# Kernel tuning notes

Measured on AMD Instinct MI355X. Metric: run time of the kernel, lower is better.

## Reference

```python
import jax, jax.numpy as jnp
import numpy as np

N, D_IN, D_OUT, Q_DIM = 4096, 256, 256, 64


def _xavier(key, shape):
    fan_in, fan_out = shape[-2], shape[-1]
    bound = float(np.sqrt(6.0 / (fan_in + fan_out)))
    return jax.random.uniform(key, shape, jnp.float32, -bound, bound)


def setup_inputs() -> dict:
    key = jax.random.key(0)
    k_x, k_q, k_w, k_b = jax.random.split(key, 4)
    x = jax.random.normal(k_x, (N, D_IN), jnp.float32)
    query_vectors = jax.random.normal(k_q, (N, Q_DIM), jnp.float32)
    W_1 = _xavier(k_w, (Q_DIM, D_IN, D_OUT))  # xavier over last two dims (matches torch on 3D)
    b_1 = _xavier(k_b, (Q_DIM, D_OUT))
    return {"x": x, "query_vectors": query_vectors, "W_1": W_1, "b_1": b_1}


def reference(x, query_vectors, W_1, b_1):
    # Per-sample dynamic weight: W[n] = sum_d q[n,d] * W_1[d]; then x[n] @ W[n] + q[n] @ b_1.
    # Fused single contraction avoids materializing the [n, i, o] tensor; same math.
    out = jnp.einsum('ni,nd,dio->no', x, query_vectors, W_1)
    out = out + query_vectors @ b_1
    return out
```

## Files before the change

kernel.cpp:

```cpp
#include <hip/hip_runtime.h>
#include <stdint.h>


typedef _Float16 f16;
typedef f16 f16x8 __attribute__((ext_vector_type(8)));
typedef float f32x16 __attribute__((ext_vector_type(16)));

#define NROWS 4096
#define QDIM 64
#define SPLIT 8
#define MBLK 64

__device__ __forceinline__ void gl_lds16(const void* g, void* s) {
  __builtin_amdgcn_global_load_lds(
      (const __attribute__((address_space(1))) void*)(uintptr_t)g,
      (__attribute__((address_space(3))) void*)(uint32_t)(uintptr_t)s,
      16, 0, 0);
}

__global__ __launch_bounds__(256) void prep(const float* __restrict__ W,
                                            const float* __restrict__ X,
                                            const float* __restrict__ Q,
                                            const float* __restrict__ B1,
                                            f16* __restrict__ Wt,
                                            f16* __restrict__ Xt,
                                            f16* __restrict__ Qt) {
  const int b = blockIdx.x;
  const int t = threadIdx.x;
  if (b < 512) {
    const int sg = b >> 6, ic = (b >> 3) & 7, dd = b & 7;
    const int g = b + (sg ? 2 : 0);
    const int k0 = ((sg << 3) + dd) * 256 + (ic << 5);
#pragma unroll
    for (int r = 0; r < 4; ++r) {
      const int gidx = (r << 8) + t;
      const int n = gidx & 255;
      const int sh = gidx >> 8;
      f16x8 h;
#pragma unroll
      for (int j = 0; j < 8; ++j)
        h[j] = (f16)W[(size_t)(k0 + (sh << 3) + j) * 256 + n];
      *(f16x8*)(Wt + (size_t)g * 8192 + (size_t)gidx * 8) = h;
    }
  } else if (b < 640) {
    const int bb = b - 512;
    const int mb = bb >> 1, half = bb & 1;
#pragma unroll
    for (int r = 0; r < 4; ++r) {
      const int gidx = (half << 10) + (r << 8) + t;
      const int row = gidx & 63;
      const int hsic = gidx >> 6;
      const float* src = X + (size_t)((mb << 6) + row) * 256 + (hsic << 3);
      float4 a = *(const float4*)src;
      float4 c = *(const float4*)(src + 4);
      f16x8 h;
      h[0] = (f16)a.x; h[1] = (f16)a.y; h[2] = (f16)a.z; h[3] = (f16)a.w;
      h[4] = (f16)c.x; h[5] = (f16)c.y; h[6] = (f16)c.z; h[7] = (f16)c.w;
      *(f16x8*)(Xt + (size_t)mb * 16384 + (size_t)gidx * 8) = h;
    }
  } else if (b < 656) {
    const int bb = b - 640;
#pragma unroll
    for (int m = 0; m < 4; ++m) {
      const int mb = (bb << 2) + m;
#pragma unroll
      for (int r = 0; r < 2; ++r) {
        const int u = (r << 8) + t;
        const int row = u & 63;
        const int sh = u >> 6;
        const float* src = Q + (size_t)((mb << 6) + row) * QDIM + (sh << 3);
        float4 a = *(const float4*)src;
        float4 c = *(const float4*)(src + 4);
        f16x8 h;
        h[0] = (f16)a.x; h[1] = (f16)a.y; h[2] = (f16)a.z; h[3] = (f16)a.w;
        h[4] = (f16)c.x; h[5] = (f16)c.y; h[6] = (f16)c.z; h[7] = (f16)c.w;
        *(f16x8*)(Qt + (size_t)mb * 4096 + (size_t)u * 8) = h;
      }
    }
  } else {
    const int cc = b - 656;
#pragma unroll
    for (int r = 0; r < 4; ++r) {
      const int gidx = (r << 8) + t;
      const int n = gidx & 255;
      const int sh = gidx >> 8;
      f16x8 h;
#pragma unroll
      for (int j = 0; j < 8; ++j)
        h[j] = (f16)B1[(size_t)((cc << 5) + (sh << 3) + j) * 256 + n];
      *(f16x8*)(Wt + (size_t)(64 + cc) * 8192 + (size_t)gidx * 8) = h;
    }
  }
}

__global__ __launch_bounds__(256, 2) void mlp_main(const float* __restrict__ Q,
                                                   const f16* __restrict__ Wt,
                                                   const f16* __restrict__ Xt,
                                                   const f16* __restrict__ Qt,
                                                   float* __restrict__ out) {
  __shared__ f16 s_x[16384];
  __shared__ f16 s_w[4][3][2048];

  const int bid = blockIdx.x;
  const int sg = bid & 7;
  const int mb = bid >> 3;
  const int t = threadIdx.x;
  const int w = t >> 6;
  const int l = t & 63;
  const int l31 = l & 31;
  const int hf = l >> 5;
  const int chunks = (sg == 0) ? 66 : 64;
  const char* wg = (const char*)(Wt + (size_t)((sg << 6) + (sg ? 2 : 0)) * 8192);

  const char* xg = (const char*)(Xt + (size_t)mb * 16384);
  char* xs = (char*)s_x;
#pragma unroll
  for (int i = 0; i < 8; ++i) {
    const int off = (((w << 3) + i) << 10) + (l << 4);
    gl_lds16(xg + off, xs + off);
  }
  char* ws0 = (char*)&s_w[w][0][0];
#pragma unroll
  for (int c0 = 0; c0 < 2; ++c0)
#pragma unroll
    for (int i = 0; i < 4; ++i)
      gl_lds16(wg + ((size_t)c0 << 14) + (i << 12) + (w << 10) + (l << 4),
               ws0 + (c0 << 12) + (i << 10) + (l << 4));

  f16 qr[2][8];
#pragma unroll
  for (int mt = 0; mt < 2; ++mt) {
    const float* qp = Q + (size_t)((mb << 6) + (mt << 5) + l31) * QDIM + (sg << 3);
#pragma unroll
    for (int dd = 0; dd < 8; ++dd) qr[mt][dd] = (f16)qp[dd];
  }

  f16x8 qf[2][2][2];
  if (sg == 0) {
#pragma unroll
    for (int cc = 0; cc < 2; ++cc)
#pragma unroll
      for (int mt = 0; mt < 2; ++mt)
#pragma unroll
        for (int s = 0; s < 2; ++s)
          qf[cc][mt][s] = *(const f16x8*)(Qt + (size_t)mb * 4096 +
              (size_t)(((((cc << 1) + s) << 1) + hf) * 64 + (mt << 5) + l31) * 8);
  }

  f32x16 acc[2][2];
#pragma unroll
  for (int a = 0; a < 2; ++a)
#pragma unroll
    for (int bq = 0; bq < 2; ++bq)
#pragma unroll
      for (int r = 0; r < 16; ++r) acc[a][bq][r] = 0.f;

  __syncthreads();

  const int wrd = (hf << 10) + (l31 << 4);
  const char* rb = ws0;
  const char* pb = ws0 + 4096;
  char* fb = ws0 + 8192;
  int pc = 2;

  for (int ic = 0; ic < 8; ++ic) {
    f16x8 xf[2][2];
#pragma unroll
    for (int s = 0; s < 2; ++s)
#pragma unroll
      for (int mt = 0; mt < 2; ++mt)
        xf[mt][s] = *(const f16x8*)(s_x +
            ((((ic << 2) + (s << 1) + hf) << 6) + (mt << 5) + l31) * 8);
#pragma unroll
    for (int dd = 0; dd < 8; ++dd) {
      const char* src = wg + ((size_t)pc << 14);
#pragma unroll
      for (int i = 0; i < 4; ++i)
        gl_lds16(src + (i << 12) + (w << 10) + (l << 4),
                 fb + (i << 10) + (l << 4));
      pc = (pc + 1 < chunks) ? pc + 1 : 0;
      const f16 qa0 = qr[0][dd], qa1 = qr[1][dd];
      f16x8 a00 = xf[0][0] * qa0, a10 = xf[1][0] * qa1;
      f16x8 a01 = xf[0][1] * qa0, a11 = xf[1][1] * qa1;
      __builtin_amdgcn_s_waitcnt(0x0F78);
      __builtin_amdgcn_sched_barrier(0);
      f16x8 bf00 = *(const f16x8*)(rb + wrd);
      f16x8 bf01 = *(const f16x8*)(rb + wrd + (1 << 9));
      f16x8 bf10 = *(const f16x8*)(rb + (2 << 10) + wrd);
      f16x8 bf11 = *(const f16x8*)(rb + (2 << 10) + wrd + (1 << 9));
      acc[0][0] = __builtin_amdgcn_mfma_f32_32x32x16_f16(a00, bf00, acc[0][0], 0, 0, 0);
      acc[1][0] = __builtin_amdgcn_mfma_f32_32x32x16_f16(a10, bf00, acc[1][0], 0, 0, 0);
      acc[0][1] = __builtin_amdgcn_mfma_f32_32x32x16_f16(a00, bf01, acc[0][1], 0, 0, 0);
      acc[1][1] = __builtin_amdgcn_mfma_f32_32x32x16_f16(a10, bf01, acc[1][1], 0, 0, 0);
      acc[0][0] = __builtin_amdgcn_mfma_f32_32x32x16_f16(a01, bf10, acc[0][0], 0, 0, 0);
      acc[1][0] = __builtin_amdgcn_mfma_f32_32x32x16_f16(a11, bf10, acc[1][0], 0, 0, 0);
      acc[0][1] = __builtin_amdgcn_mfma_f32_32x32x16_f16(a01, bf11, acc[0][1], 0, 0, 0);
      acc[1][1] = __builtin_amdgcn_mfma_f32_32x32x16_f16(a11, bf11, acc[1][1], 0, 0, 0);
      const char* tmp = rb; rb = pb; pb = fb; fb = (char*)tmp;
    }
  }

  if (sg == 0) {
#pragma unroll
    for (int cc = 0; cc < 2; ++cc) {
      const char* src = wg + ((size_t)pc << 14);
#pragma unroll
      for (int i = 0; i < 4; ++i)
        gl_lds16(src + (i << 12) + (w << 10) + (l << 4),
                 fb + (i << 10) + (l << 4));
      pc = (pc + 1 < chunks) ? pc + 1 : 0;
      __builtin_amdgcn_s_waitcnt(0x0F78);
      __builtin_amdgcn_sched_barrier(0);
      f16x8 bf00 = *(const f16x8*)(rb + wrd);
      f16x8 bf01 = *(const f16x8*)(rb + wrd + (1 << 9));
      f16x8 bf10 = *(const f16x8*)(rb + (2 << 10) + wrd);
      f16x8 bf11 = *(const f16x8*)(rb + (2 << 10) + wrd + (1 << 9));
      acc[0][0] = __builtin_amdgcn_mfma_f32_32x32x16_f16(qf[cc][0][0], bf00, acc[0][0], 0, 0, 0);
      acc[1][0] = __builtin_amdgcn_mfma_f32_32x32x16_f16(qf[cc][1][0], bf00, acc[1][0], 0, 0, 0);
      acc[0][1] = __builtin_amdgcn_mfma_f32_32x32x16_f16(qf[cc][0][0], bf01, acc[0][1], 0, 0, 0);
      acc[1][1] = __builtin_amdgcn_mfma_f32_32x32x16_f16(qf[cc][1][0], bf01, acc[1][1], 0, 0, 0);
      acc[0][0] = __builtin_amdgcn_mfma_f32_32x32x16_f16(qf[cc][0][1], bf10, acc[0][0], 0, 0, 0);
      acc[1][0] = __builtin_amdgcn_mfma_f32_32x32x16_f16(qf[cc][1][1], bf10, acc[1][0], 0, 0, 0);
      acc[0][1] = __builtin_amdgcn_mfma_f32_32x32x16_f16(qf[cc][0][1], bf11, acc[0][1], 0, 0, 0);
      acc[1][1] = __builtin_amdgcn_mfma_f32_32x32x16_f16(qf[cc][1][1], bf11, acc[1][1], 0, 0, 0);
      const char* tmp = rb; rb = pb; pb = fb; fb = (char*)tmp;
    }
  }

  __builtin_amdgcn_s_waitcnt(0x0F70);

#pragma unroll
  for (int mt = 0; mt < 2; ++mt) {
#pragma unroll
    for (int nt = 0; nt < 2; ++nt) {
#pragma unroll
      for (int r = 0; r < 16; ++r) {
        const int row = (mb << 6) + (mt << 5) + (r & 3) + ((r >> 2) << 3) + (hf << 2);
        const int col = (w << 6) + (nt << 5) + l31;
        atomicAdd(out + (size_t)row * 256 + col, acc[mt][nt][r]);
      }
    }
  }
}

extern "C" void kernel_launch(void* const* d_in, const int* in_sizes, int n_in,
                              void* d_out, int out_size, void* d_ws, size_t ws_size,
                              hipStream_t stream) {
  (void)in_sizes; (void)n_in; (void)out_size; (void)ws_size;
  const float* x  = (const float*)d_in[0];
  const float* q  = (const float*)d_in[1];
  const float* W1 = (const float*)d_in[2];
  const float* b1 = (const float*)d_in[3];
  float* out = (float*)d_out;

  f16* Wt = (f16*)d_ws;
  f16* Xt = (f16*)((char*)d_ws + (size_t)514 * 16384);
  f16* Qt = (f16*)((char*)d_ws + (size_t)514 * 16384 + (size_t)64 * 32768);

  hipMemsetAsync(out, 0, (size_t)NROWS * 256 * sizeof(float), stream);
  prep<<<658, 256, 0, stream>>>(W1, x, q, b1, Wt, Xt, Qt);
  mlp_main<<<(NROWS / MBLK) * SPLIT, 256, 0, stream>>>(q, Wt, Xt, Qt, out);
}
```

Baseline: 132.5 us.

## Load W and X fragments directly to registers, dropping LDS staging

Removes the shared-memory staging of X and W chunks (global_load_lds with triple buffering and waitcnt) and loads the MFMA operand fragments straight from global memory into registers. It uses a register double-buffer for W and for X, and raises launch bounds to 3 blocks per SM since no LDS is used. This cuts LDS traffic and explicit sync, and relies on the compiler and cache hierarchy to hide global latency. The trade-off is higher register pressure and dependence on L2/L1 for reuse of X across loops.

```diff
diff --git a/kernel.cpp b/kernel.cpp
--- a/kernel.cpp
+++ b/kernel.cpp
@@ -10,13 +10,6 @@
 #define QDIM 64
 #define SPLIT 8
 #define MBLK 64
-
-__device__ __forceinline__ void gl_lds16(const void* g, void* s) {
-  __builtin_amdgcn_global_load_lds(
-      (const __attribute__((address_space(1))) void*)(uintptr_t)g,
-      (__attribute__((address_space(3))) void*)(uint32_t)(uintptr_t)s,
-      16, 0, 0);
-}
 
 __global__ __launch_bounds__(256) void prep(const float* __restrict__ W,
                                             const float* __restrict__ X,
@@ -93,14 +86,55 @@
   }
 }
 
-__global__ __launch_bounds__(256, 2) void mlp_main(const float* __restrict__ Q,
+#define LOADW(D, P)                          \
+  do {                                       \
+    D[0] = *(const f16x8*)((P));             \
+    D[1] = *(const f16x8*)((P) + 512);       \
+    D[2] = *(const f16x8*)((P) + 8192);      \
+    D[3] = *(const f16x8*)((P) + 8704);      \
+  } while (0)
+
+#define LOADX(D, IC)                               \
+  do {                                             \
+    const char* xb_ = xg + ((IC) << 12);           \
+    D[0] = *(const f16x8*)(xb_);                   \
+    D[1] = *(const f16x8*)(xb_ + 512);             \
+    D[2] = *(const f16x8*)(xb_ + 2048);            \
+    D[3] = *(const f16x8*)(xb_ + 2560);            \
+  } while (0)
+
+#define MFMA8(XF, DD, WW)                                                        \
+  do {                                                                           \
+    const f16 q0_ = qr[0][DD], q1_ = qr[1][DD];                                  \
+    f16x8 a00_ = XF[0] * q0_, a10_ = XF[1] * q1_;                                \
+    f16x8 a01_ = XF[2] * q0_, a11_ = XF[3] * q1_;                                \
+    acc[0][0] = __builtin_amdgcn_mfma_f32_32x32x16_f16(a00_, WW[0], acc[0][0], 0, 0, 0); \
+    acc[1][0] = __builtin_amdgcn_mfma_f32_32x32x16_f16(a10_, WW[0], acc[1][0], 0, 0, 0); \
+    acc[0][1] = __builtin_amdgcn_mfma_f32_32x32x16_f16(a00_, WW[1], acc[0][1], 0, 0, 0); \
+    acc[1][1] = __builtin_amdgcn_mfma_f32_32x32x16_f16(a10_, WW[1], acc[1][1], 0, 0, 0); \
+    acc[0][0] = __builtin_amdgcn_mfma_f32_32x32x16_f16(a01_, WW[2], acc[0][0], 0, 0, 0); \
+    acc[1][0] = __builtin_amdgcn_mfma_f32_32x32x16_f16(a11_, WW[2], acc[1][0], 0, 0, 0); \
+    acc[0][1] = __builtin_amdgcn_mfma_f32_32x32x16_f16(a01_, WW[3], acc[0][1], 0, 0, 0); \
+    acc[1][1] = __builtin_amdgcn_mfma_f32_32x32x16_f16(a11_, WW[3], acc[1][1], 0, 0, 0); \
+  } while (0)
+
+#define MFMA8Q(QF, WW)                                                           \
+  do {                                                                           \
+    acc[0][0] = __builtin_amdgcn_mfma_f32_32x32x16_f16(QF[0], WW[0], acc[0][0], 0, 0, 0); \
+    acc[1][0] = __builtin_amdgcn_mfma_f32_32x32x16_f16(QF[1], WW[0], acc[1][0], 0, 0, 0); \
+    acc[0][1] = __builtin_amdgcn_mfma_f32_32x32x16_f16(QF[0], WW[1], acc[0][1], 0, 0, 0); \
+    acc[1][1] = __builtin_amdgcn_mfma_f32_32x32x16_f16(QF[1], WW[1], acc[1][1], 0, 0, 0); \
+    acc[0][0] = __builtin_amdgcn_mfma_f32_32x32x16_f16(QF[2], WW[2], acc[0][0], 0, 0, 0); \
+    acc[1][0] = __builtin_amdgcn_mfma_f32_32x32x16_f16(QF[3], WW[2], acc[1][0], 0, 0, 0); \
+    acc[0][1] = __builtin_amdgcn_mfma_f32_32x32x16_f16(QF[2], WW[3], acc[0][1], 0, 0, 0); \
+    acc[1][1] = __builtin_amdgcn_mfma_f32_32x32x16_f16(QF[3], WW[3], acc[1][1], 0, 0, 0); \
+  } while (0)
+
+__global__ __launch_bounds__(256, 3) void mlp_main(const float* __restrict__ Q,
                                                    const f16* __restrict__ Wt,
                                                    const f16* __restrict__ Xt,
                                                    const f16* __restrict__ Qt,
                                                    float* __restrict__ out) {
-  __shared__ f16 s_x[16384];
-  __shared__ f16 s_w[4][3][2048];
-
   const int bid = blockIdx.x;
   const int sg = bid & 7;
   const int mb = bid >> 3;
@@ -109,23 +143,12 @@
   const int l = t & 63;
   const int l31 = l & 31;
   const int hf = l >> 5;
-  const int chunks = (sg == 0) ? 66 : 64;
+
   const char* wg = (const char*)(Wt + (size_t)((sg << 6) + (sg ? 2 : 0)) * 8192);
-
-  const char* xg = (const char*)(Xt + (size_t)mb * 16384);
-  char* xs = (char*)s_x;
-#pragma unroll
-  for (int i = 0; i < 8; ++i) {
-    const int off = (((w << 3) + i) << 10) + (l << 4);
-    gl_lds16(xg + off, xs + off);
-  }
-  char* ws0 = (char*)&s_w[w][0][0];
-#pragma unroll
-  for (int c0 = 0; c0 < 2; ++c0)
-#pragma unroll
-    for (int i = 0; i < 4; ++i)
-      gl_lds16(wg + ((size_t)c0 << 14) + (i << 12) + (w << 10) + (l << 4),
-               ws0 + (c0 << 12) + (i << 10) + (l << 4));
+  const int wl = (hf << 12) + (w << 10) + (l31 << 4);
+  const char* cp = wg + wl;
+
+  const char* xg = (const char*)Xt + ((size_t)mb << 15) + (hf << 10) + (l31 << 4);
 
   f16 qr[2][8];
 #pragma unroll
@@ -135,99 +158,53 @@
     for (int dd = 0; dd < 8; ++dd) qr[mt][dd] = (f16)qp[dd];
   }
 
-  f16x8 qf[2][2][2];
+  f32x16 acc[2][2];
+#pragma unroll
+  for (int a = 0; a < 2; ++a)
+#pragma unroll
+    for (int bq = 0; bq < 2; ++bq)
+#pragma unroll
+      for (int r = 0; r < 16; ++r) acc[a][bq][r] = 0.f;
+
+  f16x8 WA[4], WB[4], xfA[4], xfB[4];
+
+  LOADW(WA, cp);
+  LOADX(xfA, 0);
+
+  for (int ic2 = 0; ic2 < 4; ++ic2) {
+    LOADX(xfB, (ic2 << 1) + 1);
+#pragma unroll
+    for (int p = 0; p < 4; ++p) {
+      LOADW(WB, cp + 16384);
+      MFMA8(xfA, (p << 1), WA);
+      LOADW(WA, cp + 32768);
+      MFMA8(xfA, (p << 1) + 1, WB);
+      cp += 32768;
+    }
+    LOADX(xfA, ((ic2 << 1) + 2) & 7);
+#pragma unroll
+    for (int p = 0; p < 4; ++p) {
+      LOADW(WB, cp + 16384);
+      MFMA8(xfB, (p << 1), WA);
+      LOADW(WA, cp + 32768);
+      MFMA8(xfB, (p << 1) + 1, WB);
+      cp += 32768;
+    }
+  }
+
   if (sg == 0) {
-#pragma unroll
-    for (int cc = 0; cc < 2; ++cc)
-#pragma unroll
-      for (int mt = 0; mt < 2; ++mt)
-#pragma unroll
-        for (int s = 0; s < 2; ++s)
-          qf[cc][mt][s] = *(const f16x8*)(Qt + (size_t)mb * 4096 +
-              (size_t)(((((cc << 1) + s) << 1) + hf) * 64 + (mt << 5) + l31) * 8);
-  }
-
-  f32x16 acc[2][2];
-#pragma unroll
-  for (int a = 0; a < 2; ++a)
-#pragma unroll
-    for (int bq = 0; bq < 2; ++bq)
-#pragma unroll
-      for (int r = 0; r < 16; ++r) acc[a][bq][r] = 0.f;
-
-  __syncthreads();
-
-  const int wrd = (hf << 10) + (l31 << 4);
-  const char* rb = ws0;
-  const char* pb = ws0 + 4096;
-  char* fb = ws0 + 8192;
-  int pc = 2;
-
-  for (int ic = 0; ic < 8; ++ic) {
-    f16x8 xf[2][2];
-#pragma unroll
-    for (int s = 0; s < 2; ++s)
-#pragma unroll
-      for (int mt = 0; mt < 2; ++mt)
-        xf[mt][s] = *(const f16x8*)(s_x +
-            ((((ic << 2) + (s << 1) + hf) << 6) + (mt << 5) + l31) * 8);
-#pragma unroll
-    for (int dd = 0; dd < 8; ++dd) {
-      const char* src = wg + ((size_t)pc << 14);
-#pragma unroll
-      for (int i = 0; i < 4; ++i)
-        gl_lds16(src + (i << 12) + (w << 10) + (l << 4),
-                 fb + (i << 10) + (l << 4));
-      pc = (pc + 1 < chunks) ? pc + 1 : 0;
-      const f16 qa0 = qr[0][dd], qa1 = qr[1][dd];
-      f16x8 a00 = xf[0][0] * qa0, a10 = xf[1][0] * qa1;
-      f16x8 a01 = xf[0][1] * qa0, a11 = xf[1][1] * qa1;
-      __builtin_amdgcn_s_waitcnt(0x0F78);
-      __builtin_amdgcn_sched_barrier(0);
-      f16x8 bf00 = *(const f16x8*)(rb + wrd);
-      f16x8 bf01 = *(const f16x8*)(rb + wrd + (1 << 9));
-      f16x8 bf10 = *(const f16x8*)(rb + (2 << 10) + wrd);
-      f16x8 bf11 = *(const f16x8*)(rb + (2 << 10) + wrd + (1 << 9));
-      acc[0][0] = __builtin_amdgcn_mfma_f32_32x32x16_f16(a00, bf00, acc[0][0], 0, 0, 0);
-      acc[1][0] = __builtin_amdgcn_mfma_f32_32x32x16_f16(a10, bf00, acc[1][0], 0, 0, 0);
-      acc[0][1] = __builtin_amdgcn_mfma_f32_32x32x16_f16(a00, bf01, acc[0][1], 0, 0, 0);
-      acc[1][1] = __builtin_amdgcn_mfma_f32_32x32x16_f16(a10, bf01, acc[1][1], 0, 0, 0);
-      acc[0][0] = __builtin_amdgcn_mfma_f32_32x32x16_f16(a01, bf10, acc[0][0], 0, 0, 0);
-      acc[1][0] = __builtin_amdgcn_mfma_f32_32x32x16_f16(a11, bf10, acc[1][0], 0, 0, 0);
-      acc[0][1] = __builtin_amdgcn_mfma_f32_32x32x16_f16(a01, bf11, acc[0][1], 0, 0, 0);
-      acc[1][1] = __builtin_amdgcn_mfma_f32_32x32x16_f16(a11, bf11, acc[1][1], 0, 0, 0);
-      const char* tmp = rb; rb = pb; pb = fb; fb = (char*)tmp;
-    }
-  }
-
-  if (sg == 0) {
-#pragma unroll
-    for (int cc = 0; cc < 2; ++cc) {
-      const char* src = wg + ((size_t)pc << 14);
-#pragma unroll
-      for (int i = 0; i < 4; ++i)
-        gl_lds16(src + (i << 12) + (w << 10) + (l << 4),
-                 fb + (i << 10) + (l << 4));
-      pc = (pc + 1 < chunks) ? pc + 1 : 0;
-      __builtin_amdgcn_s_waitcnt(0x0F78);
-      __builtin_amdgcn_sched_barrier(0);
-      f16x8 bf00 = *(const f16x8*)(rb + wrd);
-      f16x8 bf01 = *(const f16x8*)(rb + wrd + (1 << 9));
-      f16x8 bf10 = *(const f16x8*)(rb + (2 << 10) + wrd);
-      f16x8 bf11 = *(const f16x8*)(rb + (2 << 10) + wrd + (1 << 9));
-      acc[0][0] = __builtin_amdgcn_mfma_f32_32x32x16_f16(qf[cc][0][0], bf00, acc[0][0], 0, 0, 0);
-      acc[1][0] = __builtin_amdgcn_mfma_f32_32x32x16_f16(qf[cc][1][0], bf00, acc[1][0], 0, 0, 0);
-      acc[0][1] = __builtin_amdgcn_mfma_f32_32x32x16_f16(qf[cc][0][0], bf01, acc[0][1], 0, 0, 0);
-      acc[1][1] = __builtin_amdgcn_mfma_f32_32x32x16_f16(qf[cc][1][0], bf01, acc[1][1], 0, 0, 0);
-      acc[0][0] = __builtin_amdgcn_mfma_f32_32x32x16_f16(qf[cc][0][1], bf10, acc[0][0], 0, 0, 0);
-      acc[1][0] = __builtin_amdgcn_mfma_f32_32x32x16_f16(qf[cc][1][1], bf10, acc[1][0], 0, 0, 0);
-      acc[0][1] = __builtin_amdgcn_mfma_f32_32x32x16_f16(qf[cc][0][1], bf11, acc[0][1], 0, 0, 0);
-      acc[1][1] = __builtin_amdgcn_mfma_f32_32x32x16_f16(qf[cc][1][1], bf11, acc[1][1], 0, 0, 0);
-      const char* tmp = rb; rb = pb; pb = fb; fb = (char*)tmp;
-    }
-  }
-
-  __builtin_amdgcn_s_waitcnt(0x0F70);
+    LOADW(WB, cp + 16384);
+    f16x8 QF0[4], QF1[4];
+    const char* qg = (const char*)Qt + ((size_t)mb << 13) + (hf << 10) + (l31 << 4);
+#pragma unroll
+    for (int u = 0; u < 4; ++u)
+      QF0[u] = *(const f16x8*)(qg + ((u >> 1) << 11) + ((u & 1) << 9));
+#pragma unroll
+    for (int u = 0; u < 4; ++u)
+      QF1[u] = *(const f16x8*)(qg + 4096 + ((u >> 1) << 11) + ((u & 1) << 9));
+    MFMA8Q(QF0, WA);
+    MFMA8Q(QF1, WB);
+  }
 
 #pragma unroll
   for (int mt = 0; mt < 2; ++mt) {
```

New measurement: 147.2 us. 1.11x slower.
